# Kernel tuning notes

Measured on AMD Instinct MI355X. Metric: run time of the kernel, lower is better.

The kernel has to match this reference:

```python
import jax, jax.numpy as jnp
import numpy as np

B, T, U = 4, 256, 128
EH, PH, JH, V = 1024, 640, 640, 1024


def setup_inputs() -> dict:
    key = jax.random.key(0)
    ks = jax.random.split(key, 8)
    s_e = 1.0 / np.sqrt(EH)
    s_p = 1.0 / np.sqrt(PH)
    s_j = 1.0 / np.sqrt(JH)
    return {
        "enc": jax.random.normal(ks[0], (B, EH, T), jnp.float32),
        "dec": jax.random.normal(ks[1], (B, PH, U), jnp.float32),
        "W_enc": jax.random.uniform(ks[2], (JH, EH), jnp.float32, -s_e, s_e),
        "b_enc": jax.random.uniform(ks[3], (JH,), jnp.float32, -s_e, s_e),
        "W_pred": jax.random.uniform(ks[4], (JH, PH), jnp.float32, -s_p, s_p),
        "b_pred": jax.random.uniform(ks[5], (JH,), jnp.float32, -s_p, s_p),
        "W_out": jax.random.uniform(ks[6], (V, JH), jnp.float32, -s_j, s_j),
        "b_out": jax.random.uniform(ks[7], (V,), jnp.float32, -s_j, s_j),
    }


def reference(enc, dec, W_enc, b_enc, W_pred, b_pred, W_out, b_out):
    # enc: [B, EH, T], dec: [B, PH, U]  (channels-first, as in torch forward)
    # enc projection -> [B, T, JH] (transpose fused into einsum)
    e = jnp.einsum('bht,jh->btj', enc, W_enc) + b_enc
    # pred projection -> [B, U, JH]
    p = jnp.einsum('bhu,jh->buj', dec, W_pred) + b_pred
    # broadcast add -> [B, T, U, JH], ReLU, output projection -> [B, T, U, V]
    h = jax.nn.relu(e[:, :, None, :] + p[:, None, :, :])
    logits = jnp.einsum('btuj,vj->btuv', h, W_out) + b_out
    return jax.nn.log_softmax(logits, axis=-1)
```

## Files before the change

kernel.cpp:

```cpp
#include <hip/hip_runtime.h>
#include <hip/hip_bf16.h>
#include <stdint.h>

#define B_ 4
#define T_ 256
#define U_ 128
#define EH_ 1024
#define PH_ 640
#define JH_ 640
#define V_ 1024
#define KT_ 20

typedef short bf16x8 __attribute__((ext_vector_type(8)));
typedef float f32x4 __attribute__((ext_vector_type(4)));
typedef unsigned short u16;

typedef const __attribute__((address_space(1))) uint32_t cgu32_t;
typedef __attribute__((address_space(3))) uint32_t lu32_t;

__device__ __forceinline__ u16 f2bf(float f) {
  union { float f; uint32_t u; } v;
  v.f = f;
  uint32_t u = v.u;
  return (u16)((u + 0x7FFFu + ((u >> 16) & 1u)) >> 16);
}

__device__ __forceinline__ uint32_t cvt2(float lo, float hi) {
  uint32_t r;
  asm("v_cvt_pk_bf16_f32 %0, %1, %2" : "=v"(r) : "v"(lo), "v"(hi));
  return r;
}

__device__ __forceinline__ void gload16(const void* g, void* l) {
  __builtin_amdgcn_global_load_lds((cgu32_t*)g, (lu32_t*)l, 16, 0, 0);
}

#define VMW(n) asm volatile("s_waitcnt vmcnt(" #n ")" ::: "memory")
#define LGKM0  asm volatile("s_waitcnt lgkmcnt(0)" ::: "memory")
#define SCHEDB __builtin_amdgcn_sched_barrier(0)

__global__ void k_transpose_cvt(const float* __restrict__ in, u16* __restrict__ out,
                                int H, int W) {
  __shared__ float tile[32][33];
  int b = blockIdx.z;
  int h0 = blockIdx.y * 32, w0 = blockIdx.x * 32;
  const float* pin = in + (size_t)b * H * W;
  u16* pout = out + (size_t)b * H * W;
  int lw = threadIdx.x & 31, lh = threadIdx.x >> 5;
#pragma unroll
  for (int i = 0; i < 4; i++) {
    int h = lh + i * 8;
    tile[h][lw] = pin[(size_t)(h0 + h) * W + (w0 + lw)];
  }
  __syncthreads();
#pragma unroll
  for (int i = 0; i < 4; i++) {
    int w = lh + i * 8;
    pout[(size_t)(w0 + w) * H + (h0 + lw)] = f2bf(tile[lw][w]);
  }
}

__global__ void k_prep_w(const float* __restrict__ We, const float* __restrict__ Wp,
                         const float* __restrict__ Wo,
                         u16* __restrict__ WeB, u16* __restrict__ WpB,
                         u16* __restrict__ Wpk) {
  int s = blockIdx.x * 256 + threadIdx.x;
  if (s < 163840) {
    int idx = s * 4;
    float4 v = *(const float4*)(We + idx);
    ushort4 o;
    o.x = f2bf(v.x); o.y = f2bf(v.y); o.z = f2bf(v.z); o.w = f2bf(v.w);
    *(ushort4*)(WeB + idx) = o;
  } else if (s < 266240) {
    int idx = (s - 163840) * 4;
    float4 v = *(const float4*)(Wp + idx);
    ushort4 o;
    o.x = f2bf(v.x); o.y = f2bf(v.y); o.z = f2bf(v.z); o.w = f2bf(v.w);
    *(ushort4*)(WpB + idx) = o;
  } else {
    int q = s - 266240;
    int c = q & 1023;
    int g = (q >> 10) & 3;
    int t = q >> 12;
    const float* src = Wo + (size_t)c * JH_ + t * 32 + g * 8;
    float4 a = *(const float4*)src;
    float4 b2 = *(const float4*)(src + 4);
    ushort4 lo, hi;
    lo.x = f2bf(a.x);  lo.y = f2bf(a.y);  lo.z = f2bf(a.z);  lo.w = f2bf(a.w);
    hi.x = f2bf(b2.x); hi.y = f2bf(b2.y); hi.z = f2bf(b2.z); hi.w = f2bf(b2.w);
    u16* d = Wpk + (size_t)q * 8;
    *(ushort4*)d = lo;
    *(ushort4*)(d + 4) = hi;
  }
}

__global__ void k_proj_gemm(const u16* __restrict__ A, const u16* __restrict__ Bm,
                            const float* __restrict__ bias, float* __restrict__ C,
                            int K, int N, size_t strideA, size_t strideC) {
  __shared__ __align__(16) u16 sA[64 * 64];
  __shared__ __align__(16) u16 sB[64 * 64];
  int bb = blockIdx.z;
  const u16* Ab = A + (size_t)bb * strideA;
  float* Cb = C + (size_t)bb * strideC;
  int m0 = blockIdx.x * 64, n0 = blockIdx.y * 64;
  int tid = threadIdx.x;
  int lane = tid & 63, wid = tid >> 6;

  f32x4 acc[2][2] = {};
  for (int kk = 0; kk < K; kk += 64) {
#pragma unroll
    for (int i = 0; i < 2; i++) {
      int c = tid + i * 256;
      int r = c >> 3, kc = c & 7;
      int s = (r << 3) | (kc ^ (r & 7));
      *(bf16x8*)(sA + s * 8) = *(const bf16x8*)(Ab + (size_t)(m0 + r) * K + kk + kc * 8);
      *(bf16x8*)(sB + s * 8) = *(const bf16x8*)(Bm + (size_t)(n0 + r) * K + kk + kc * 8);
    }
    __syncthreads();
    int wr = (wid >> 1) * 32, wc = (wid & 1) * 32;
    int lr = lane & 15, lk = lane >> 4;
#pragma unroll
    for (int ki = 0; ki < 2; ki++) {
      bf16x8 af[2], bq[2];
#pragma unroll
      for (int mf = 0; mf < 2; mf++) {
        int r = wr + mf * 16 + lr;
        int kc = ki * 4 + lk;
        int s = (r << 3) | (kc ^ (r & 7));
        af[mf] = *(const bf16x8*)(sA + s * 8);
      }
#pragma unroll
      for (int nf = 0; nf < 2; nf++) {
        int r = wc + nf * 16 + lr;
        int kc = ki * 4 + lk;
        int s = (r << 3) | (kc ^ (r & 7));
        bq[nf] = *(const bf16x8*)(sB + s * 8);
      }
#pragma unroll
      for (int mf = 0; mf < 2; mf++)
#pragma unroll
        for (int nf = 0; nf < 2; nf++)
          acc[mf][nf] = __builtin_amdgcn_mfma_f32_16x16x32_bf16(af[mf], bq[nf], acc[mf][nf], 0, 0, 0);
    }
    __syncthreads();
  }
  int wr = (wid >> 1) * 32, wc = (wid & 1) * 32;
  int lr = lane & 15, lq = lane >> 4;
#pragma unroll
  for (int nf = 0; nf < 2; nf++) {
    int n = n0 + wc + nf * 16 + lr;
    float bv = bias[n];
#pragma unroll
    for (int mf = 0; mf < 2; mf++) {
#pragma unroll
      for (int r = 0; r < 4; r++) {
        int m = m0 + wr + mf * 16 + lq * 4 + r;
        Cb[(size_t)m * N + n] = acc[mf][nf][r] + bv;
      }
    }
  }
}

__global__ void k_pack_p2(const float* __restrict__ pBuf, float* __restrict__ pPk) {
  int s = blockIdx.x * 256 + threadIdx.x;
  int bh = s / 10240;
  int rem = s - bh * 10240;
  int g4 = rem >> 6;
  int r = rem & 63;
  int b = bh >> 1, half = bh & 1;
  const float* src = pBuf + ((size_t)(b * 128 + half * 64 + r)) * JH_ + g4 * 4;
  float4 v = *(const float4*)src;
  *(float4*)(pPk + (size_t)s * 4) = v;
}

__global__ __launch_bounds__(512)
void k_fused3(const float* __restrict__ e, const float* __restrict__ pPk,
              const u16* __restrict__ Wpk, const float* __restrict__ bout,
              float* __restrict__ out) {
  __shared__ __align__(16) u16 sB[2][32768];
  __shared__ __align__(16) u16 sA[2][4096];
  __shared__ __align__(16) float sE[JH_];
  __shared__ float redm[512];
  __shared__ float reds[512];

  int bid = blockIdx.x;
  int btile = bid >> 1, half = bid & 1, b = btile >> 8;
  int tid = threadIdx.x, lane = tid & 63, wn = tid >> 6;
  int lr = lane & 15, lk = lane >> 4;
  int ph = (bid % 10) * 2;

  const float* eRow = e + (size_t)btile * JH_;
  const float* pPbase = pPk + ((size_t)(b * 2 + half) * 40960) + wn * 256 + lane * 4;
  float* outB = out + ((size_t)btile * U_ + half * 64) * V_;

  int awr = (wn >> 1) * 512 + lane * 8 + (wn & 1) * 4;

  f32x4 acc[4][8] = {};

  auto tp = [&](int t) { int x = t + ph; return x >= KT_ ? x - KT_ : x; };
  auto stage = [&](int tph, int c) {
    const u16* s0 = Wpk + (size_t)tph * 32768 + (2 * wn) * 512 + lane * 8;
    u16* d0 = &sB[c][(2 * wn) * 512];
#pragma unroll
    for (int g = 0; g < 4; g++) {
      gload16(s0 + g * 8192, d0 + g * 8192);
      gload16(s0 + g * 8192 + 512, d0 + g * 8192 + 512);
    }
  };
  auto loadp = [&](int tph) { return *(const float4*)(pPbase + tph * 2048); };
  auto build = [&](int slot, int tin, int tph, float4 pv) {
    float4 ev = *(const float4*)(&sE[tph * 32 + wn * 4]);
    uint2 w;
    w.x = cvt2(fmaxf(pv.x + ev.x, 0.f), fmaxf(pv.y + ev.y, 0.f));
    w.y = cvt2(fmaxf(pv.z + ev.z, 0.f), fmaxf(pv.w + ev.w, 0.f));
    *(uint2*)(&sA[slot][tin * 2048 + awr]) = w;
  };

  for (int i = tid; i < JH_; i += 512) sE[i] = eRow[i];
  stage(tp(0), 0);
  float4 p0  = loadp(tp(0));
  float4 p1  = loadp(tp(1));
  float4 pcA = loadp(tp(2));
  float4 pcB = loadp(tp(3));
  float4 pnA = p0, pnB = p0;
  LGKM0;
  __builtin_amdgcn_s_barrier();
  build(0, 0, tp(0), p0);
  build(0, 1, tp(1), p1);
  asm volatile("s_waitcnt vmcnt(0) lgkmcnt(0)" ::: "memory");
  __builtin_amdgcn_s_barrier();

#pragma unroll
  for (int t = 0; t < KT_; t++) {
    if (t + 1 < KT_) stage(tp(t + 1), (t + 1) & 1);
    if ((t & 1) == 0 && t + 4 < KT_) { pnA = loadp(tp(t + 4)); pnB = loadp(tp(t + 5)); }
    if ((t & 1) == 0 && t + 2 < KT_) {
      int q1 = ((t >> 1) + 1) & 1;
      build(q1, 0, tp(t + 2), pcA);
      build(q1, 1, tp(t + 3), pcB);
    }
    SCHEDB;
    if (t <= 15) { VMW(10); } else if (t <= 18) { VMW(8); } else { VMW(0); }
    SCHEDB;
    const u16* Ab = &sA[(t >> 1) & 1][(t & 1) * 2048 + lk * 512];
    const u16* Bb = &sB[t & 1][lk * 8192 + wn * 1024];
    bf16x8 af[4], bq[8];
#pragma unroll
    for (int mf = 0; mf < 4; mf++)
      af[mf] = *(const bf16x8*)(Ab + (mf * 16 + lr) * 8);
#pragma unroll
    for (int nf = 0; nf < 8; nf++)
      bq[nf] = *(const bf16x8*)(Bb + (nf * 16 + lr) * 8);
    LGKM0; SCHEDB;
    __builtin_amdgcn_s_setprio(1);
#pragma unroll
    for (int mf = 0; mf < 4; mf++)
#pragma unroll
      for (int nf = 0; nf < 8; nf++)
        acc[mf][nf] = __builtin_amdgcn_mfma_f32_16x16x32_bf16(af[mf], bq[nf], acc[mf][nf], 0, 0, 0);
    __builtin_amdgcn_s_setprio(0);
    if ((t & 1) && t + 1 < KT_) {
      pcA = pnA; pcB = pnB;
      LGKM0;
      __builtin_amdgcn_s_barrier();
    }
  }

  float bv[8];
#pragma unroll
  for (int nf = 0; nf < 8; nf++) bv[nf] = bout[wn * 128 + nf * 16 + lr];
#pragma unroll
  for (int mf = 0; mf < 4; mf++)
#pragma unroll
    for (int nf = 0; nf < 8; nf++)
#pragma unroll
      for (int r = 0; r < 4; r++)
        acc[mf][nf][r] += bv[nf];

  float gm[4][4];
#pragma unroll
  for (int mf = 0; mf < 4; mf++)
#pragma unroll
    for (int r = 0; r < 4; r++) {
      float m = acc[mf][0][r];
#pragma unroll
      for (int nf = 1; nf < 8; nf++) m = fmaxf(m, acc[mf][nf][r]);
#pragma unroll
      for (int o = 1; o < 16; o <<= 1) m = fmaxf(m, __shfl_xor(m, o, 64));
      gm[mf][r] = m;
    }
  if ((lane & 15) == 0) {
#pragma unroll
    for (int mf = 0; mf < 4; mf++)
#pragma unroll
      for (int r = 0; r < 4; r++)
        redm[(mf * 16 + lk * 4 + r) * 8 + wn] = gm[mf][r];
  }
  __syncthreads();
#pragma unroll
  for (int mf = 0; mf < 4; mf++)
#pragma unroll
    for (int r = 0; r < 4; r++) {
      int row = mf * 16 + lk * 4 + r;
      float m = redm[row * 8];
#pragma unroll
      for (int w = 1; w < 8; w++) m = fmaxf(m, redm[row * 8 + w]);
      gm[mf][r] = m;
    }
  float ls[4][4];
#pragma unroll
  for (int mf = 0; mf < 4; mf++)
#pragma unroll
    for (int r = 0; r < 4; r++) {
      float s = 0.f;
#pragma unroll
      for (int nf = 0; nf < 8; nf++) s += __expf(acc[mf][nf][r] - gm[mf][r]);
#pragma unroll
      for (int o = 1; o < 16; o <<= 1) s += __shfl_xor(s, o, 64);
      ls[mf][r] = s;
    }
  if ((lane & 15) == 0) {
#pragma unroll
    for (int mf = 0; mf < 4; mf++)
#pragma unroll
      for (int r = 0; r < 4; r++)
        reds[(mf * 16 + lk * 4 + r) * 8 + wn] = ls[mf][r];
  }
  __syncthreads();
#pragma unroll
  for (int mf = 0; mf < 4; mf++)
#pragma unroll
    for (int r = 0; r < 4; r++) {
      int row = mf * 16 + lk * 4 + r;
      float s = reds[row * 8];
#pragma unroll
      for (int w = 1; w < 8; w++) s += reds[row * 8 + w];
      ls[mf][r] = gm[mf][r] + __logf(s);
    }
#pragma unroll
  for (int mf = 0; mf < 4; mf++)
#pragma unroll
    for (int nf = 0; nf < 8; nf++)
#pragma unroll
      for (int r = 0; r < 4; r++)
        outB[(size_t)(mf * 16 + lk * 4 + r) * V_ + wn * 128 + nf * 16 + lr] =
            acc[mf][nf][r] - ls[mf][r];
}

extern "C" void kernel_launch(void* const* d_in, const int* in_sizes, int n_in,
                              void* d_out, int out_size, void* d_ws, size_t ws_size,
                              hipStream_t stream) {
  const float* enc    = (const float*)d_in[0];
  const float* dec    = (const float*)d_in[1];
  const float* W_enc  = (const float*)d_in[2];
  const float* b_enc  = (const float*)d_in[3];
  const float* W_pred = (const float*)d_in[4];
  const float* b_pred = (const float*)d_in[5];
  const float* W_out  = (const float*)d_in[6];
  const float* b_out  = (const float*)d_in[7];
  float* out = (float*)d_out;

  char* ws = (char*)d_ws;
  size_t off = 0;
  auto alloc = [&](size_t bytes) {
    void* pp = ws + off;
    off = (off + bytes + 255) & ~(size_t)255;
    return pp;
  };
  u16* encT   = (u16*)alloc((size_t)B_ * T_ * EH_ * 2);
  u16* decT   = (u16*)alloc((size_t)B_ * U_ * PH_ * 2);
  u16* WencB  = (u16*)alloc((size_t)JH_ * EH_ * 2);
  u16* WpredB = (u16*)alloc((size_t)JH_ * PH_ * 2);
  u16* Wpk    = (u16*)alloc((size_t)KT_ * 32768 * 2);
  float* eBuf = (float*)alloc((size_t)B_ * T_ * JH_ * 4);
  float* pBuf = (float*)alloc((size_t)B_ * U_ * JH_ * 4);
  float* pPk  = (float*)alloc((size_t)81920 * 4 * 4);

  k_transpose_cvt<<<dim3(T_ / 32, EH_ / 32, B_), 256, 0, stream>>>(enc, encT, EH_, T_);
  k_transpose_cvt<<<dim3(U_ / 32, PH_ / 32, B_), 256, 0, stream>>>(dec, decT, PH_, U_);
  k_prep_w<<<1360, 256, 0, stream>>>(W_enc, W_pred, W_out, WencB, WpredB, Wpk);
  k_proj_gemm<<<dim3(T_ / 64, JH_ / 64, B_), 256, 0, stream>>>(
      encT, WencB, b_enc, eBuf, EH_, JH_, (size_t)T_ * EH_, (size_t)T_ * JH_);
  k_proj_gemm<<<dim3(U_ / 64, JH_ / 64, B_), 256, 0, stream>>>(
      decT, WpredB, b_pred, pBuf, PH_, JH_, (size_t)U_ * PH_, (size_t)U_ * JH_);
  k_pack_p2<<<320, 256, 0, stream>>>(pBuf, pPk);

  k_fused3<<<B_ * T_ * 2, 512, 0, stream>>>(eBuf, pPk, Wpk, b_out, out);
}
```

Baseline: 312.7 us.

## Load W_out fragments directly from global into registers instead of LDS staging

The fused output-projection kernel no longer stages W_out tiles into a 128KB LDS double buffer through global_load_lds. Each wave now loads its own B fragments straight from global memory into a double-buffered register array, one K-step ahead. This drops a large LDS allocation, which may allow more blocks per CU, and removes the LDS read traffic plus the manual waitcnt and sched_barrier choreography. In exchange it raises register pressure and leaves the compiler to place the waits, so global load latency may be hidden less well.

```diff
diff --git a/kernel.cpp b/kernel.cpp
--- a/kernel.cpp
+++ b/kernel.cpp
@@ -15,9 +15,6 @@
 typedef float f32x4 __attribute__((ext_vector_type(4)));
 typedef unsigned short u16;
 
-typedef const __attribute__((address_space(1))) uint32_t cgu32_t;
-typedef __attribute__((address_space(3))) uint32_t lu32_t;
-
 __device__ __forceinline__ u16 f2bf(float f) {
   union { float f; uint32_t u; } v;
   v.f = f;
@@ -31,13 +28,7 @@
   return r;
 }
 
-__device__ __forceinline__ void gload16(const void* g, void* l) {
-  __builtin_amdgcn_global_load_lds((cgu32_t*)g, (lu32_t*)l, 16, 0, 0);
-}
-
-#define VMW(n) asm volatile("s_waitcnt vmcnt(" #n ")" ::: "memory")
 #define LGKM0  asm volatile("s_waitcnt lgkmcnt(0)" ::: "memory")
-#define SCHEDB __builtin_amdgcn_sched_barrier(0)
 
 __global__ void k_transpose_cvt(const float* __restrict__ in, u16* __restrict__ out,
                                 int H, int W) {
@@ -174,10 +165,9 @@
 }
 
 __global__ __launch_bounds__(512)
-void k_fused3(const float* __restrict__ e, const float* __restrict__ pPk,
+void k_fused4(const float* __restrict__ e, const float* __restrict__ pPk,
               const u16* __restrict__ Wpk, const float* __restrict__ bout,
               float* __restrict__ out) {
-  __shared__ __align__(16) u16 sB[2][32768];
   __shared__ __align__(16) u16 sA[2][4096];
   __shared__ __align__(16) float sE[JH_];
   __shared__ float redm[512];
@@ -191,21 +181,19 @@
 
   const float* eRow = e + (size_t)btile * JH_;
   const float* pPbase = pPk + ((size_t)(b * 2 + half) * 40960) + wn * 256 + lane * 4;
+  const u16* wB = Wpk + ((size_t)lk * 1024 + wn * 128 + lr) * 8;
   float* outB = out + ((size_t)btile * U_ + half * 64) * V_;
 
   int awr = (wn >> 1) * 512 + lane * 8 + (wn & 1) * 4;
 
   f32x4 acc[4][8] = {};
+  bf16x8 bq[2][8];
 
   auto tp = [&](int t) { int x = t + ph; return x >= KT_ ? x - KT_ : x; };
-  auto stage = [&](int tph, int c) {
-    const u16* s0 = Wpk + (size_t)tph * 32768 + (2 * wn) * 512 + lane * 8;
-    u16* d0 = &sB[c][(2 * wn) * 512];
-#pragma unroll
-    for (int g = 0; g < 4; g++) {
-      gload16(s0 + g * 8192, d0 + g * 8192);
-      gload16(s0 + g * 8192 + 512, d0 + g * 8192 + 512);
-    }
+  auto loadB = [&](int tph, bf16x8* d) {
+#pragma unroll
+    for (int nf = 0; nf < 8; nf++)
+      d[nf] = *(const bf16x8*)(wB + (size_t)tph * 32768 + nf * 128);
   };
   auto loadp = [&](int tph) { return *(const float4*)(pPbase + tph * 2048); };
   auto build = [&](int slot, int tin, int tph, float4 pv) {
@@ -216,8 +204,8 @@
     *(uint2*)(&sA[slot][tin * 2048 + awr]) = w;
   };
 
+  loadB(tp(0), bq[0]);
   for (int i = tid; i < JH_; i += 512) sE[i] = eRow[i];
-  stage(tp(0), 0);
   float4 p0  = loadp(tp(0));
   float4 p1  = loadp(tp(1));
   float4 pcA = loadp(tp(2));
@@ -227,37 +215,31 @@
   __builtin_amdgcn_s_barrier();
   build(0, 0, tp(0), p0);
   build(0, 1, tp(1), p1);
-  asm volatile("s_waitcnt vmcnt(0) lgkmcnt(0)" ::: "memory");
+  LGKM0;
   __builtin_amdgcn_s_barrier();
 
 #pragma unroll
   for (int t = 0; t < KT_; t++) {
-    if (t + 1 < KT_) stage(tp(t + 1), (t + 1) & 1);
-    if ((t & 1) == 0 && t + 4 < KT_) { pnA = loadp(tp(t + 4)); pnB = loadp(tp(t + 5)); }
-    if ((t & 1) == 0 && t + 2 < KT_) {
-      int q1 = ((t >> 1) + 1) & 1;
-      build(q1, 0, tp(t + 2), pcA);
-      build(q1, 1, tp(t + 3), pcB);
-    }
-    SCHEDB;
-    if (t <= 15) { VMW(10); } else if (t <= 18) { VMW(8); } else { VMW(0); }
-    SCHEDB;
+    if (t + 1 < KT_) loadB(tp(t + 1), bq[(t + 1) & 1]);
+    if ((t & 1) == 0) {
+      if (t + 4 < KT_) { pnA = loadp(tp(t + 4)); pnB = loadp(tp(t + 5)); }
+      if (t + 2 < KT_) {
+        int q1 = ((t >> 1) + 1) & 1;
+        build(q1, 0, tp(t + 2), pcA);
+        build(q1, 1, tp(t + 3), pcB);
+      }
+    }
     const u16* Ab = &sA[(t >> 1) & 1][(t & 1) * 2048 + lk * 512];
-    const u16* Bb = &sB[t & 1][lk * 8192 + wn * 1024];
-    bf16x8 af[4], bq[8];
+    bf16x8 af[4];
 #pragma unroll
     for (int mf = 0; mf < 4; mf++)
       af[mf] = *(const bf16x8*)(Ab + (mf * 16 + lr) * 8);
-#pragma unroll
-    for (int nf = 0; nf < 8; nf++)
-      bq[nf] = *(const bf16x8*)(Bb + (nf * 16 + lr) * 8);
-    LGKM0; SCHEDB;
     __builtin_amdgcn_s_setprio(1);
 #pragma unroll
     for (int mf = 0; mf < 4; mf++)
 #pragma unroll
       for (int nf = 0; nf < 8; nf++)
-        acc[mf][nf] = __builtin_amdgcn_mfma_f32_16x16x32_bf16(af[mf], bq[nf], acc[mf][nf], 0, 0, 0);
+        acc[mf][nf] = __builtin_amdgcn_mfma_f32_16x16x32_bf16(af[mf], bq[t & 1][nf], acc[mf][nf], 0, 0, 0);
     __builtin_amdgcn_s_setprio(0);
     if ((t & 1) && t + 1 < KT_) {
       pcA = pnA; pcB = pnB;
@@ -385,5 +367,5 @@
       decT, WpredB, b_pred, pBuf, PH_, JH_, (size_t)U_ * PH_, (size_t)U_ * JH_);
   k_pack_p2<<<320, 256, 0, stream>>>(pBuf, pPk);
 
-  k_fused3<<<B_ * T_ * 2, 512, 0, stream>>>(eBuf, pPk, Wpk, b_out, out);
-}
+  k_fused4<<<B_ * T_ * 2, 512, 0, stream>>>(eBuf, pPk, Wpk, b_out, out);
+}
```

Result: faster. 298.9 us (-4.4%).
